# Optimization experiments

Measured on AMD Instinct MI355X. Metric: run time of the kernel, lower is better.

## Reference

```python
import jax, jax.numpy as jnp
import numpy as np

K = 3  # dynamic filter kernel size
EPS = 1e-10


def _filter_norm_spatial(s, std_param):
    # s: (B, K*K, H, W); normalize over filter-tap dim (unbiased std, as torch)
    s = s - s.mean(axis=1, keepdims=True)
    s = s / (s.std(axis=1, keepdims=True, ddof=1) + EPS)
    return s * std_param[None, :, None, None]


def _filter_norm_channel(cf, std_param, B, C):
    # cf: (B, C*K*K); normalize over the K*K taps of each channel
    cf = cf.reshape(B, C, K * K)
    cf = cf - cf.mean(axis=2, keepdims=True)
    cf = cf / (cf.std(axis=2, keepdims=True, ddof=1) + EPS)
    cf = cf.reshape(B, C * K * K) * std_param[None, :]
    return cf.reshape(B, C, K * K)


def _ddf_pack(x, sw, sb, sstd, cw1, cb1, cw2, cb2, cstd):
    B, C, H, W = x.shape
    # spatial branch: 1x1 conv -> per-pixel K*K spatial filter
    s = jnp.einsum('bchw,oc->bohw', x, sw) + sb[None, :, None, None]
    s = _filter_norm_spatial(s, sstd)                      # (B, 9, H, W)
    # channel branch: GAP -> SE MLP -> per-channel K*K filter
    g = x.mean(axis=(2, 3))                                # (B, C)
    h = jax.nn.relu(g @ cw1.T + cb1)                       # (B, mid)
    cf = h @ cw2.T + cb2                                   # (B, C*9)
    cf = _filter_norm_channel(cf, cstd, B, C)              # (B, C, 9)
    # apply decoupled dynamic filter: w[b,c,uv,h,w] = cf[b,c,uv] * s[b,uv,h,w]
    pad = K // 2
    xp = jnp.pad(x, ((0, 0), (0, 0), (pad, pad), (pad, pad)))
    # patches: (B, C, 9, H, W) -- the 9 shifted views (unfold)
    patches = jnp.stack([xp[:, :, i:i + H, j:j + W]
                         for i in range(K) for j in range(K)], axis=2)
    return jnp.einsum('bckhw,bck,bkhw->bchw', patches, cf, s)


def setup_inputs() -> dict:
    key = jax.random.key(0)
    ks = jax.random.split(key, 20)
    nf, mid = 64, 12
    std_scale = np.sqrt(2.0) / K  # calculate_gain('relu') / kernel_size
    d = {'x': jax.random.normal(ks[0], (4, nf, 256, 256), jnp.float32)}
    i = 1
    for p in ('1', '2'):
        d['sw' + p] = jax.random.normal(ks[i], (K * K, nf), jnp.float32) * 0.1; i += 1
        d['sb' + p] = jax.random.normal(ks[i], (K * K,), jnp.float32) * 0.1; i += 1
        d['sstd' + p] = jax.random.normal(ks[i], (K * K,), jnp.float32) * std_scale; i += 1
        d['cw1_' + p] = jax.random.normal(ks[i], (mid, nf), jnp.float32) * 0.1; i += 1
        d['cb1_' + p] = jax.random.normal(ks[i], (mid,), jnp.float32) * 0.1; i += 1
        d['cw2_' + p] = jax.random.normal(ks[i], (nf * K * K, mid), jnp.float32) * 0.1; i += 1
        d['cb2_' + p] = jax.random.normal(ks[i], (nf * K * K,), jnp.float32) * 0.1; i += 1
        d['cstd' + p] = jax.random.normal(ks[i], (nf * K * K,), jnp.float32) * std_scale; i += 1
    return d


def reference(x, sw1, sb1, sstd1, cw1_1, cb1_1, cw2_1, cb2_1, cstd1,
              sw2, sb2, sstd2, cw1_2, cb1_2, cw2_2, cb2_2, cstd2):
    out = _ddf_pack(x, sw1, sb1, sstd1, cw1_1, cb1_1, cw2_1, cb2_1, cstd1)
    out = jax.nn.relu(out)
    out = _ddf_pack(out, sw2, sb2, sstd2, cw1_2, cb1_2, cw2_2, cb2_2, cstd2)
    return x + out
```

## Files before the change

kernel.cpp:

```cpp
#include <hip/hip_runtime.h>

#define B_ 4
#define C_ 64
#define H_ 256
#define W_ 256
#define HW_ (H_*W_)
#define MID_ 12
#define NPB_ 128

__device__ __forceinline__ float wave_reduce64(float v) {
#pragma unroll
    for (int off = 32; off; off >>= 1) v += __shfl_xor(v, off, 64);
    return v;
}

__device__ __forceinline__ void fnorm9(float* t9, const float* __restrict__ sstd) {
    float mean = 0.f;
#pragma unroll
    for (int t = 0; t < 9; ++t) mean += t9[t];
    mean *= (1.f / 9.f);
    float var = 0.f;
#pragma unroll
    for (int t = 0; t < 9; ++t) { float d = t9[t] - mean; var += d * d; }
    float inv = 1.f / (sqrtf(var * (1.f / 8.f)) + 1e-10f);
#pragma unroll
    for (int t = 0; t < 9; ++t) t9[t] = (t9[t] - mean) * inv * sstd[t];
}

__global__ __launch_bounds__(256) void prep_kernel(const float* __restrict__ x,
    const float* __restrict__ sw, const float* __restrict__ sb,
    const float* __restrict__ sstd, float* __restrict__ sarr, float* __restrict__ gp) {
    const int tid = threadIdx.x;
    const int lane = tid & 63, wv = tid >> 6;
    const int col0 = (blockIdx.x * 64 + lane) * 2;
    const int row  = blockIdx.y * 4 + wv;
    const int b = blockIdx.z;
    __shared__ float lg[4][C_];

    float st0[9], st1[9];
#pragma unroll
    for (int t = 0; t < 9; ++t) { float bb = sb[t]; st0[t] = bb; st1[t] = bb; }

    const float* xp = x + ((size_t)b * C_) * HW_ + (size_t)row * W_ + col0;
    for (int c = 0; c < C_; ++c) {
        float2 v = *(const float2*)(xp + (size_t)c * HW_);
#pragma unroll
        for (int t = 0; t < 9; ++t) {
            float wt = sw[t * C_ + c];
            st0[t] = fmaf(v.x, wt, st0[t]);
            st1[t] = fmaf(v.y, wt, st1[t]);
        }
        float gs = wave_reduce64(v.x + v.y);
        if (lane == 0) lg[wv][c] = gs;
    }
    fnorm9(st0, sstd);
    fnorm9(st1, sstd);
    {
        float* sp = sarr + ((size_t)b * 9) * HW_ + (size_t)row * W_ + col0;
#pragma unroll
        for (int t = 0; t < 9; ++t)
            *(float2*)(sp + (size_t)t * HW_) = make_float2(st0[t], st1[t]);
    }
    __syncthreads();
    if (tid < C_) {
        float s4 = lg[0][tid] + lg[1][tid] + lg[2][tid] + lg[3][tid];
        gp[((size_t)b * C_ + tid) * NPB_ + blockIdx.y * gridDim.x + blockIdx.x] = s4;
    }
}

__global__ __launch_bounds__(256) void cfk(const float* __restrict__ gp,
    const float* __restrict__ cw1, const float* __restrict__ cb1,
    const float* __restrict__ cw2, const float* __restrict__ cb2,
    const float* __restrict__ cstd, float* __restrict__ cf) {
    const int tid = threadIdx.x;
    const int b = tid >> 6, c = tid & 63;
    __shared__ float gsm[B_][C_];
    __shared__ float hsm[B_][MID_];
    {
        const float4* p4 = (const float4*)(gp + ((size_t)b * C_ + c) * NPB_);
        float s = 0.f;
#pragma unroll
        for (int i = 0; i < NPB_ / 4; ++i) { float4 v = p4[i]; s += (v.x + v.y) + (v.z + v.w); }
        gsm[b][c] = s * (1.f / HW_);
    }
    __syncthreads();
    if (tid < B_ * MID_) {
        int b2 = tid / MID_, m = tid % MID_;
        float a = cb1[m];
        for (int cc = 0; cc < C_; ++cc) a = fmaf(gsm[b2][cc], cw1[m * C_ + cc], a);
        hsm[b2][m] = fmaxf(a, 0.f);
    }
    __syncthreads();
    float v[9];
    float mean = 0.f;
#pragma unroll
    for (int t = 0; t < 9; ++t) {
        int o = c * 9 + t;
        float a = cb2[o];
#pragma unroll
        for (int m = 0; m < MID_; ++m) a = fmaf(hsm[b][m], cw2[o * MID_ + m], a);
        v[t] = a;
        mean += a;
    }
    mean *= (1.f / 9.f);
    float var = 0.f;
#pragma unroll
    for (int t = 0; t < 9; ++t) { float d = v[t] - mean; var += d * d; }
    float inv = 1.f / (sqrtf(var * (1.f / 8.f)) + 1e-10f);
#pragma unroll
    for (int t = 0; t < 9; ++t)
        cf[((size_t)b * C_ + c) * 9 + t] = (v[t] - mean) * inv * cstd[c * 9 + t];
}

template<bool PASS1>
__global__ __launch_bounds__(256) void apply_kernel(const float* __restrict__ in,
    const float* __restrict__ sarr, const float* __restrict__ cf,
    const float* __restrict__ swn, const float* __restrict__ sbn,
    const float* __restrict__ sstdn, const float* __restrict__ resid,
    float* __restrict__ out, float* __restrict__ snext, float* __restrict__ gpn) {
    const int tid = threadIdx.x;
    const int lane = tid & 63, wv = tid >> 6;
    const int col0 = (blockIdx.x * 64 + lane) * 2;
    const int row  = blockIdx.y * 4 + wv;
    int b, c0, cN;
    if (PASS1) { b = blockIdx.z; c0 = 0; cN = C_; }
    else       { b = blockIdx.z >> 1; c0 = (blockIdx.z & 1) * (C_ / 2); cN = C_ / 2; }
    __shared__ float lg[4][C_];

    float s0[9], s1[9];
    {
        const float* sp = sarr + ((size_t)b * 9) * HW_ + (size_t)row * W_ + col0;
#pragma unroll
        for (int t = 0; t < 9; ++t) {
            float2 v = *(const float2*)(sp + (size_t)t * HW_);
            s0[t] = v.x; s1[t] = v.y;
        }
    }
    float nt0[9], nt1[9];
    if (PASS1) {
#pragma unroll
        for (int t = 0; t < 9; ++t) { float bb = sbn[t]; nt0[t] = bb; nt1[t] = bb; }
    }

    const bool rup = row > 0, rdn = row < H_ - 1;
    const bool cl = col0 > 0, cr = (col0 + 2) < W_;
    const size_t pix = (size_t)row * W_ + col0;
    const float* base = in + ((size_t)b * C_ + c0) * HW_ + pix;
    const float* cfb  = cf + ((size_t)b * C_ + c0) * 9;
    float* outp = out + ((size_t)b * C_ + c0) * HW_ + pix;
    const float* rbase = PASS1 ? nullptr : (resid + ((size_t)b * C_ + c0) * HW_ + pix);

    for (int c = 0; c < cN; ++c) {
        const float* p = base + (size_t)c * HW_;
        float m[3][4];
#pragma unroll
        for (int dr = 0; dr < 3; ++dr) {
            const float* rp = p + (dr - 1) * W_;
            const bool rv = (dr == 0) ? rup : ((dr == 2) ? rdn : true);
            float2 mid = rv ? *(const float2*)rp : make_float2(0.f, 0.f);
            m[dr][1] = mid.x; m[dr][2] = mid.y;
            m[dr][0] = (rv && cl) ? rp[-1] : 0.f;
            m[dr][3] = (rv && cr) ? rp[2] : 0.f;
        }
        float acc0 = 0.f, acc1 = 0.f;
#pragma unroll
        for (int dr = 0; dr < 3; ++dr)
#pragma unroll
            for (int dc = 0; dc < 3; ++dc) {
                const int t = dr * 3 + dc;
                const float w = cfb[c * 9 + t];
                acc0 = fmaf(m[dr][dc]     * s0[t], w, acc0);
                acc1 = fmaf(m[dr][dc + 1] * s1[t], w, acc1);
            }
        float2 o;
        if (PASS1) {
            o.x = fmaxf(acc0, 0.f);
            o.y = fmaxf(acc1, 0.f);
#pragma unroll
            for (int t = 0; t < 9; ++t) {
                float wt = swn[t * C_ + c];
                nt0[t] = fmaf(o.x, wt, nt0[t]);
                nt1[t] = fmaf(o.y, wt, nt1[t]);
            }
            float gs = wave_reduce64(o.x + o.y);
            if (lane == 0) lg[wv][c] = gs;
        } else {
            float2 rv = *(const float2*)(rbase + (size_t)c * HW_);
            o.x = acc0 + rv.x;
            o.y = acc1 + rv.y;
        }
        *(float2*)(outp + (size_t)c * HW_) = o;
    }

    if (PASS1) {
        fnorm9(nt0, sstdn);
        fnorm9(nt1, sstdn);
        float* sp = snext + ((size_t)b * 9) * HW_ + pix;
#pragma unroll
        for (int t = 0; t < 9; ++t)
            *(float2*)(sp + (size_t)t * HW_) = make_float2(nt0[t], nt1[t]);
        __syncthreads();
        if (tid < C_) {
            float s4 = lg[0][tid] + lg[1][tid] + lg[2][tid] + lg[3][tid];
            gpn[((size_t)b * C_ + tid) * NPB_ + blockIdx.y * gridDim.x + blockIdx.x] = s4;
        }
    }
}

__global__ __launch_bounds__(256) void gap_kernel(const float* __restrict__ in,
                                                  float* __restrict__ g) {
    int bc = blockIdx.x;
    const float4* p4 = (const float4*)(in + (size_t)bc * HW_);
    float sum = 0.f;
    for (int i = threadIdx.x; i < HW_ / 4; i += 256) {
        float4 v = p4[i];
        sum += (v.x + v.y) + (v.z + v.w);
    }
    __shared__ float red[256];
    red[threadIdx.x] = sum;
    __syncthreads();
    for (int s = 128; s > 0; s >>= 1) {
        if (threadIdx.x < s) red[threadIdx.x] += red[threadIdx.x + s];
        __syncthreads();
    }
    if (threadIdx.x == 0) g[bc] = red[0] * (1.0f / HW_);
}

__global__ __launch_bounds__(256) void cf_kernel(const float* __restrict__ g,
    const float* __restrict__ cw1, const float* __restrict__ cb1,
    const float* __restrict__ cw2, const float* __restrict__ cb2,
    const float* __restrict__ cstd, float* __restrict__ cf) {
    __shared__ float hsm[B_][MID_];
    int tid = threadIdx.x;
    if (tid < B_ * MID_) {
        int b = tid / MID_, m = tid % MID_;
        float acc = cb1[m];
        for (int c = 0; c < C_; ++c) acc = fmaf(g[b * C_ + c], cw1[m * C_ + c], acc);
        hsm[b][m] = fmaxf(acc, 0.f);
    }
    __syncthreads();
    int b = tid >> 6, c = tid & 63;
    float v[9];
    float mean = 0.f;
#pragma unroll
    for (int t = 0; t < 9; ++t) {
        int o = c * 9 + t;
        float acc = cb2[o];
#pragma unroll
        for (int m = 0; m < MID_; ++m) acc = fmaf(hsm[b][m], cw2[o * MID_ + m], acc);
        v[t] = acc;
        mean += acc;
    }
    mean *= (1.f / 9.f);
    float var = 0.f;
#pragma unroll
    for (int t = 0; t < 9; ++t) { float d = v[t] - mean; var += d * d; }
    float inv = 1.f / (sqrtf(var * (1.f / 8.f)) + 1e-10f);
#pragma unroll
    for (int t = 0; t < 9; ++t)
        cf[(b * C_ + c) * 9 + t] = (v[t] - mean) * inv * cstd[c * 9 + t];
}

template <bool RELU, bool RESID>
__global__ __launch_bounds__(256) void ddf_main(const float* __restrict__ in,
    const float* __restrict__ sw, const float* __restrict__ sb,
    const float* __restrict__ sstd, const float* __restrict__ cf,
    const float* __restrict__ resid, float* __restrict__ out) {
    const int tx = threadIdx.x & 63, ty = threadIdx.x >> 6;
    const int w = blockIdx.x * 64 + tx;
    const int h = blockIdx.y * 4 + ty;
    const int b = blockIdx.z;
    const float* xb = in + (size_t)b * C_ * HW_;
    float s[9];
#pragma unroll
    for (int t = 0; t < 9; ++t) s[t] = sb[t];
    {
        const float* xp = xb + h * W_ + w;
        for (int c = 0; c < C_; ++c) {
            float xv = xp[(size_t)c * HW_];
#pragma unroll
            for (int t = 0; t < 9; ++t) s[t] = fmaf(xv, sw[t * C_ + c], s[t]);
        }
    }
    float mean = 0.f;
#pragma unroll
    for (int t = 0; t < 9; ++t) mean += s[t];
    mean *= (1.f / 9.f);
    float var = 0.f;
#pragma unroll
    for (int t = 0; t < 9; ++t) { float d = s[t] - mean; var += d * d; }
    float inv = 1.f / (sqrtf(var * (1.f / 8.f)) + 1e-10f);
#pragma unroll
    for (int t = 0; t < 9; ++t) s[t] = (s[t] - mean) * inv * sstd[t];
    const bool rok0 = (h > 0), rok2 = (h < H_ - 1);
    const bool cok0 = (w > 0), cok2 = (w < W_ - 1);
    const float* cfb = cf + b * (C_ * 9);
    const size_t base = (size_t)h * W_ + w;
    const size_t bbase = (size_t)b * C_ * HW_ + base;
    for (int c = 0; c < C_; ++c) {
        const float* xc = xb + (size_t)c * HW_ + base;
        float acc = 0.f;
#pragma unroll
        for (int i = 0; i < 3; ++i) {
            const bool rok = (i == 0) ? rok0 : ((i == 2) ? rok2 : true);
#pragma unroll
            for (int j = 0; j < 3; ++j) {
                const bool cok = (j == 0) ? cok0 : ((j == 2) ? cok2 : true);
                float xv = (rok && cok) ? xc[(i - 1) * W_ + (j - 1)] : 0.f;
                acc = fmaf(xv, cfb[c * 9 + i * 3 + j] * s[i * 3 + j], acc);
            }
        }
        if (RELU) acc = fmaxf(acc, 0.f);
        size_t oidx = bbase + (size_t)c * HW_;
        if (RESID) acc += resid[oidx];
        out[oidx] = acc;
    }
}

extern "C" void kernel_launch(void* const* d_in, const int* in_sizes, int n_in,
                              void* d_out, int out_size, void* d_ws, size_t ws_size,
                              hipStream_t stream) {
    const float* x     = (const float*)d_in[0];
    const float* sw1   = (const float*)d_in[1];
    const float* sb1   = (const float*)d_in[2];
    const float* sstd1 = (const float*)d_in[3];
    const float* cw1_1 = (const float*)d_in[4];
    const float* cb1_1 = (const float*)d_in[5];
    const float* cw2_1 = (const float*)d_in[6];
    const float* cb2_1 = (const float*)d_in[7];
    const float* cstd1 = (const float*)d_in[8];
    const float* sw2   = (const float*)d_in[9];
    const float* sb2   = (const float*)d_in[10];
    const float* sstd2 = (const float*)d_in[11];
    const float* cw1_2 = (const float*)d_in[12];
    const float* cb1_2 = (const float*)d_in[13];
    const float* cw2_2 = (const float*)d_in[14];
    const float* cb2_2 = (const float*)d_in[15];
    const float* cstd2 = (const float*)d_in[16];
    float* outp = (float*)d_out;

    const size_t n_out1 = (size_t)B_ * C_ * HW_;
    const size_t n_s    = (size_t)B_ * 9 * HW_;
    const size_t n_cf   = (size_t)B_ * C_ * 9;
    const size_t n_gp   = (size_t)B_ * C_ * NPB_;
    const size_t need_new = (n_out1 + 2 * n_s + 2 * n_cf + 2 * n_gp) * sizeof(float);

    if (ws_size >= need_new) {
        float* out1 = (float*)d_ws;
        float* s1   = out1 + n_out1;
        float* s2   = s1 + n_s;
        float* cf1  = s2 + n_s;
        float* cf2  = cf1 + n_cf;
        float* gp1  = cf2 + n_cf;
        float* gp2  = gp1 + n_gp;

        dim3 gmain(W_ / 128, H_ / 4, B_);
        dim3 gmain2(W_ / 128, H_ / 4, B_ * 2);

        prep_kernel<<<gmain, 256, 0, stream>>>(x, sw1, sb1, sstd1, s1, gp1);
        cfk<<<1, 256, 0, stream>>>(gp1, cw1_1, cb1_1, cw2_1, cb2_1, cstd1, cf1);
        apply_kernel<true><<<gmain, 256, 0, stream>>>(x, s1, cf1, sw2, sb2, sstd2,
                                                      nullptr, out1, s2, gp2);
        cfk<<<1, 256, 0, stream>>>(gp2, cw1_2, cb1_2, cw2_2, cb2_2, cstd2, cf2);
        apply_kernel<false><<<gmain2, 256, 0, stream>>>(out1, s2, cf2, nullptr, nullptr,
                                                        nullptr, x, outp, nullptr, nullptr);
        return;
    }

    const size_t need_old = (n_out1 + 256 + n_cf) * sizeof(float);
    if (ws_size < need_old) return;
    float* out1 = (float*)d_ws;
    float* g    = out1 + n_out1;
    float* cfb  = g + 256;
    dim3 grid(W_ / 64, H_ / 4, B_);
    gap_kernel<<<B_ * C_, 256, 0, stream>>>(x, g);
    cf_kernel<<<1, 256, 0, stream>>>(g, cw1_1, cb1_1, cw2_1, cb2_1, cstd1, cfb);
    ddf_main<true, false><<<grid, 256, 0, stream>>>(x, sw1, sb1, sstd1, cfb, nullptr, out1);
    gap_kernel<<<B_ * C_, 256, 0, stream>>>(out1, g);
    cf_kernel<<<1, 256, 0, stream>>>(g, cw1_2, cb1_2, cw2_2, cb2_2, cstd2, cfb);
    ddf_main<false, true><<<grid, 256, 0, stream>>>(out1, sw2, sb2, sstd2, cfb, x, outp);
}
```

Baseline: 162.0 us.

## Split channels across waves with one pixel per thread and LDS reduction

Reworks prep and apply kernels so that each block covers one row segment of 64 pixels. Each of the four waves handles 16 channels, and the partial spatial-filter sums are combined through LDS. Channel filters are padded to 12 floats so they load as float4, and the GAP partials grow to 1024 slots written per channel per wave. This raises the block count and cuts per-thread serial channel loops, at the cost of scalar (non-float2) accesses, more GAP partial writes, and a longer cfk reduction.

After: 223.0 us. 37.7% more time.

```diff
diff --git a/kernel.cpp b/kernel.cpp
--- a/kernel.cpp
+++ b/kernel.cpp
@@ -6,7 +6,7 @@
 #define W_ 256
 #define HW_ (H_*W_)
 #define MID_ 12
-#define NPB_ 128
+#define NPB_ 1024
 
 __device__ __forceinline__ float wave_reduce64(float v) {
 #pragma unroll
@@ -30,41 +30,38 @@
 __global__ __launch_bounds__(256) void prep_kernel(const float* __restrict__ x,
     const float* __restrict__ sw, const float* __restrict__ sb,
     const float* __restrict__ sstd, float* __restrict__ sarr, float* __restrict__ gp) {
-    const int tid = threadIdx.x;
-    const int lane = tid & 63, wv = tid >> 6;
-    const int col0 = (blockIdx.x * 64 + lane) * 2;
-    const int row  = blockIdx.y * 4 + wv;
+    const int lane = threadIdx.x & 63, wv = threadIdx.x >> 6;
+    const int col = blockIdx.x * 64 + lane;
+    const int row = blockIdx.y;
     const int b = blockIdx.z;
-    __shared__ float lg[4][C_];
-
-    float st0[9], st1[9];
-#pragma unroll
-    for (int t = 0; t < 9; ++t) { float bb = sb[t]; st0[t] = bb; st1[t] = bb; }
-
-    const float* xp = x + ((size_t)b * C_) * HW_ + (size_t)row * W_ + col0;
-    for (int c = 0; c < C_; ++c) {
-        float2 v = *(const float2*)(xp + (size_t)c * HW_);
-#pragma unroll
-        for (int t = 0; t < 9; ++t) {
-            float wt = sw[t * C_ + c];
-            st0[t] = fmaf(v.x, wt, st0[t]);
-            st1[t] = fmaf(v.y, wt, st1[t]);
-        }
-        float gs = wave_reduce64(v.x + v.y);
-        if (lane == 0) lg[wv][c] = gs;
-    }
-    fnorm9(st0, sstd);
-    fnorm9(st1, sstd);
-    {
-        float* sp = sarr + ((size_t)b * 9) * HW_ + (size_t)row * W_ + col0;
+    const int c0 = wv * 16;
+    const int bslot = blockIdx.y * gridDim.x + blockIdx.x;
+    __shared__ float lds[4][9][64];
+
+    float st[9];
+#pragma unroll
+    for (int t = 0; t < 9; ++t) st[t] = 0.f;
+
+    const float* xp = x + ((size_t)b * C_ + c0) * HW_ + (size_t)row * W_ + col;
+    for (int i = 0; i < 16; ++i) {
+        float v = xp[(size_t)i * HW_];
+#pragma unroll
+        for (int t = 0; t < 9; ++t) st[t] = fmaf(v, sw[t * C_ + c0 + i], st[t]);
+        float g = wave_reduce64(v);
+        if (lane == 0) gp[((size_t)b * C_ + c0 + i) * NPB_ + bslot] = g;
+    }
+#pragma unroll
+    for (int t = 0; t < 9; ++t) lds[wv][t][lane] = st[t];
+    __syncthreads();
+    if (wv == 0) {
+        float t9[9];
 #pragma unroll
         for (int t = 0; t < 9; ++t)
-            *(float2*)(sp + (size_t)t * HW_) = make_float2(st0[t], st1[t]);
-    }
-    __syncthreads();
-    if (tid < C_) {
-        float s4 = lg[0][tid] + lg[1][tid] + lg[2][tid] + lg[3][tid];
-        gp[((size_t)b * C_ + tid) * NPB_ + blockIdx.y * gridDim.x + blockIdx.x] = s4;
+            t9[t] = sb[t] + lds[0][t][lane] + lds[1][t][lane] + lds[2][t][lane] + lds[3][t][lane];
+        fnorm9(t9, sstd);
+        float* sp = sarr + ((size_t)b * 9) * HW_ + (size_t)row * W_ + col;
+#pragma unroll
+        for (int t = 0; t < 9; ++t) sp[(size_t)t * HW_] = t9[t];
     }
 }
 
@@ -79,7 +76,6 @@
     {
         const float4* p4 = (const float4*)(gp + ((size_t)b * C_ + c) * NPB_);
         float s = 0.f;
-#pragma unroll
         for (int i = 0; i < NPB_ / 4; ++i) { float4 v = p4[i]; s += (v.x + v.y) + (v.z + v.w); }
         gsm[b][c] = s * (1.f / HW_);
     }
@@ -107,9 +103,10 @@
 #pragma unroll
     for (int t = 0; t < 9; ++t) { float d = v[t] - mean; var += d * d; }
     float inv = 1.f / (sqrtf(var * (1.f / 8.f)) + 1e-10f);
-#pragma unroll
-    for (int t = 0; t < 9; ++t)
-        cf[((size_t)b * C_ + c) * 9 + t] = (v[t] - mean) * inv * cstd[c * 9 + t];
+    float* o12 = cf + ((size_t)b * C_ + c) * 12;
+#pragma unroll
+    for (int t = 0; t < 9; ++t) o12[t] = (v[t] - mean) * inv * cstd[c * 9 + t];
+    o12[9] = 0.f; o12[10] = 0.f; o12[11] = 0.f;
 }
 
 template<bool PASS1>
@@ -118,91 +115,77 @@
     const float* __restrict__ swn, const float* __restrict__ sbn,
     const float* __restrict__ sstdn, const float* __restrict__ resid,
     float* __restrict__ out, float* __restrict__ snext, float* __restrict__ gpn) {
-    const int tid = threadIdx.x;
-    const int lane = tid & 63, wv = tid >> 6;
-    const int col0 = (blockIdx.x * 64 + lane) * 2;
-    const int row  = blockIdx.y * 4 + wv;
-    int b, c0, cN;
-    if (PASS1) { b = blockIdx.z; c0 = 0; cN = C_; }
-    else       { b = blockIdx.z >> 1; c0 = (blockIdx.z & 1) * (C_ / 2); cN = C_ / 2; }
-    __shared__ float lg[4][C_];
-
-    float s0[9], s1[9];
+    const int lane = threadIdx.x & 63, wv = threadIdx.x >> 6;
+    const int col = blockIdx.x * 64 + lane;
+    const int row = blockIdx.y;
+    const int b = blockIdx.z;
+    const int c0 = wv * 16;
+    const int bslot = blockIdx.y * gridDim.x + blockIdx.x;
+    __shared__ float lds[4][9][64];
+
+    float s0[9];
     {
-        const float* sp = sarr + ((size_t)b * 9) * HW_ + (size_t)row * W_ + col0;
-#pragma unroll
-        for (int t = 0; t < 9; ++t) {
-            float2 v = *(const float2*)(sp + (size_t)t * HW_);
-            s0[t] = v.x; s1[t] = v.y;
-        }
-    }
-    float nt0[9], nt1[9];
+        const float* sp = sarr + ((size_t)b * 9) * HW_ + (size_t)row * W_ + col;
+#pragma unroll
+        for (int t = 0; t < 9; ++t) s0[t] = sp[(size_t)t * HW_];
+    }
+    float nt[9];
     if (PASS1) {
 #pragma unroll
-        for (int t = 0; t < 9; ++t) { float bb = sbn[t]; nt0[t] = bb; nt1[t] = bb; }
+        for (int t = 0; t < 9; ++t) nt[t] = 0.f;
     }
 
     const bool rup = row > 0, rdn = row < H_ - 1;
-    const bool cl = col0 > 0, cr = (col0 + 2) < W_;
-    const size_t pix = (size_t)row * W_ + col0;
-    const float* base = in + ((size_t)b * C_ + c0) * HW_ + pix;
-    const float* cfb  = cf + ((size_t)b * C_ + c0) * 9;
-    float* outp = out + ((size_t)b * C_ + c0) * HW_ + pix;
-    const float* rbase = PASS1 ? nullptr : (resid + ((size_t)b * C_ + c0) * HW_ + pix);
-
-    for (int c = 0; c < cN; ++c) {
-        const float* p = base + (size_t)c * HW_;
-        float m[3][4];
+    const bool cl = col > 0, cr = col < W_ - 1;
+    const float* base = in + ((size_t)b * C_ + c0) * HW_ + (size_t)row * W_ + col;
+    const float* cfb  = cf + ((size_t)b * C_ + c0) * 12;
+    float* outp = out + ((size_t)b * C_ + c0) * HW_ + (size_t)row * W_ + col;
+    const float* rb = PASS1 ? nullptr : (resid + ((size_t)b * C_ + c0) * HW_ + (size_t)row * W_ + col);
+
+    for (int i = 0; i < 16; ++i) {
+        const float4* cfv = (const float4*)(cfb + (size_t)i * 12);
+        float4 ca = cfv[0], cb4 = cfv[1], cc4 = cfv[2];
+        const float cw9[9] = {ca.x, ca.y, ca.z, ca.w, cb4.x, cb4.y, cb4.z, cb4.w, cc4.x};
+        const float* p = base + (size_t)i * HW_;
+        float acc = 0.f;
 #pragma unroll
         for (int dr = 0; dr < 3; ++dr) {
+            const bool rv = (dr == 0) ? rup : ((dr == 2) ? rdn : true);
             const float* rp = p + (dr - 1) * W_;
-            const bool rv = (dr == 0) ? rup : ((dr == 2) ? rdn : true);
-            float2 mid = rv ? *(const float2*)rp : make_float2(0.f, 0.f);
-            m[dr][1] = mid.x; m[dr][2] = mid.y;
-            m[dr][0] = (rv && cl) ? rp[-1] : 0.f;
-            m[dr][3] = (rv && cr) ? rp[2] : 0.f;
-        }
-        float acc0 = 0.f, acc1 = 0.f;
-#pragma unroll
-        for (int dr = 0; dr < 3; ++dr)
-#pragma unroll
-            for (int dc = 0; dc < 3; ++dc) {
-                const int t = dr * 3 + dc;
-                const float w = cfb[c * 9 + t];
-                acc0 = fmaf(m[dr][dc]     * s0[t], w, acc0);
-                acc1 = fmaf(m[dr][dc + 1] * s1[t], w, acc1);
-            }
-        float2 o;
+            float ml = (rv && cl) ? rp[-1] : 0.f;
+            float mm = rv ? rp[0] : 0.f;
+            float mr = (rv && cr) ? rp[1] : 0.f;
+            const int t = dr * 3;
+            acc = fmaf(ml * s0[t],     cw9[t],     acc);
+            acc = fmaf(mm * s0[t + 1], cw9[t + 1], acc);
+            acc = fmaf(mr * s0[t + 2], cw9[t + 2], acc);
+        }
+        float o;
         if (PASS1) {
-            o.x = fmaxf(acc0, 0.f);
-            o.y = fmaxf(acc1, 0.f);
-#pragma unroll
-            for (int t = 0; t < 9; ++t) {
-                float wt = swn[t * C_ + c];
-                nt0[t] = fmaf(o.x, wt, nt0[t]);
-                nt1[t] = fmaf(o.y, wt, nt1[t]);
-            }
-            float gs = wave_reduce64(o.x + o.y);
-            if (lane == 0) lg[wv][c] = gs;
+            o = fmaxf(acc, 0.f);
+#pragma unroll
+            for (int t = 0; t < 9; ++t) nt[t] = fmaf(o, swn[t * C_ + c0 + i], nt[t]);
+            float g = wave_reduce64(o);
+            if (lane == 0) gpn[((size_t)b * C_ + c0 + i) * NPB_ + bslot] = g;
         } else {
-            float2 rv = *(const float2*)(rbase + (size_t)c * HW_);
-            o.x = acc0 + rv.x;
-            o.y = acc1 + rv.y;
-        }
-        *(float2*)(outp + (size_t)c * HW_) = o;
+            o = acc + rb[(size_t)i * HW_];
+        }
+        outp[(size_t)i * HW_] = o;
     }
 
     if (PASS1) {
-        fnorm9(nt0, sstdn);
-        fnorm9(nt1, sstdn);
-        float* sp = snext + ((size_t)b * 9) * HW_ + pix;
-#pragma unroll
-        for (int t = 0; t < 9; ++t)
-            *(float2*)(sp + (size_t)t * HW_) = make_float2(nt0[t], nt1[t]);
+#pragma unroll
+        for (int t = 0; t < 9; ++t) lds[wv][t][lane] = nt[t];
         __syncthreads();
-        if (tid < C_) {
-            float s4 = lg[0][tid] + lg[1][tid] + lg[2][tid] + lg[3][tid];
-            gpn[((size_t)b * C_ + tid) * NPB_ + blockIdx.y * gridDim.x + blockIdx.x] = s4;
+        if (wv == 0) {
+            float t9[9];
+#pragma unroll
+            for (int t = 0; t < 9; ++t)
+                t9[t] = sbn[t] + lds[0][t][lane] + lds[1][t][lane] + lds[2][t][lane] + lds[3][t][lane];
+            fnorm9(t9, sstdn);
+            float* sp = snext + ((size_t)b * 9) * HW_ + (size_t)row * W_ + col;
+#pragma unroll
+            for (int t = 0; t < 9; ++t) sp[(size_t)t * HW_] = t9[t];
         }
     }
 }
@@ -341,7 +324,7 @@
 
     const size_t n_out1 = (size_t)B_ * C_ * HW_;
     const size_t n_s    = (size_t)B_ * 9 * HW_;
-    const size_t n_cf   = (size_t)B_ * C_ * 9;
+    const size_t n_cf   = (size_t)B_ * C_ * 12;
     const size_t n_gp   = (size_t)B_ * C_ * NPB_;
     const size_t need_new = (n_out1 + 2 * n_s + 2 * n_cf + 2 * n_gp) * sizeof(float);
 
@@ -354,29 +337,28 @@
         float* gp1  = cf2 + n_cf;
         float* gp2  = gp1 + n_gp;
 
-        dim3 gmain(W_ / 128, H_ / 4, B_);
-        dim3 gmain2(W_ / 128, H_ / 4, B_ * 2);
-
-        prep_kernel<<<gmain, 256, 0, stream>>>(x, sw1, sb1, sstd1, s1, gp1);
+        dim3 g(W_ / 64, H_, B_);
+
+        prep_kernel<<<g, 256, 0, stream>>>(x, sw1, sb1, sstd1, s1, gp1);
         cfk<<<1, 256, 0, stream>>>(gp1, cw1_1, cb1_1, cw2_1, cb2_1, cstd1, cf1);
-        apply_kernel<true><<<gmain, 256, 0, stream>>>(x, s1, cf1, sw2, sb2, sstd2,
-                                                      nullptr, out1, s2, gp2);
+        apply_kernel<true><<<g, 256, 0, stream>>>(x, s1, cf1, sw2, sb2, sstd2,
+                                                  nullptr, out1, s2, gp2);
         cfk<<<1, 256, 0, stream>>>(gp2, cw1_2, cb1_2, cw2_2, cb2_2, cstd2, cf2);
-        apply_kernel<false><<<gmain2, 256, 0, stream>>>(out1, s2, cf2, nullptr, nullptr,
-                                                        nullptr, x, outp, nullptr, nullptr);
+        apply_kernel<false><<<g, 256, 0, stream>>>(out1, s2, cf2, nullptr, nullptr,
+                                                   nullptr, x, outp, nullptr, nullptr);
         return;
     }
 
-    const size_t need_old = (n_out1 + 256 + n_cf) * sizeof(float);
+    const size_t need_old = (n_out1 + 256 + (size_t)B_ * C_ * 9) * sizeof(float);
     if (ws_size < need_old) return;
     float* out1 = (float*)d_ws;
-    float* g    = out1 + n_out1;
-    float* cfb  = g + 256;
+    float* gg   = out1 + n_out1;
+    float* cfb  = gg + 256;
     dim3 grid(W_ / 64, H_ / 4, B_);
-    gap_kernel<<<B_ * C_, 256, 0, stream>>>(x, g);
-    cf_kernel<<<1, 256, 0, stream>>>(g, cw1_1, cb1_1, cw2_1, cb2_1, cstd1, cfb);
+    gap_kernel<<<B_ * C_, 256, 0, stream>>>(x, gg);
+    cf_kernel<<<1, 256, 0, stream>>>(gg, cw1_1, cb1_1, cw2_1, cb2_1, cstd1, cfb);
     ddf_main<true, false><<<grid, 256, 0, stream>>>(x, sw1, sb1, sstd1, cfb, nullptr, out1);
-    gap_kernel<<<B_ * C_, 256, 0, stream>>>(out1, g);
-    cf_kernel<<<1, 256, 0, stream>>>(g, cw1_2, cb1_2, cw2_2, cb2_2, cstd2, cfb);
+    gap_kernel<<<B_ * C_, 256, 0, stream>>>(out1, gg);
+    cf_kernel<<<1, 256, 0, stream>>>(gg, cw1_2, cb1_2, cw2_2, cb2_2, cstd2, cfb);
     ddf_main<false, true><<<grid, 256, 0, stream>>>(out1, sw2, sb2, sstd2, cfb, x, outp);
 }
```
